# Performance work log

Measured on AMD Instinct MI355X. Metric: run time of the kernel, lower is better.

## Reference

```python
import jax, jax.numpy as jnp
import numpy as np

B, D_MODEL, H, D_MEM, M = 512, 2048, 8, 128, 512
MAX_WRITE_FACTOR = 0.7


def act(x):
    # elu(x) + 1, the standard positive linear-attention kernel activation
    return jax.nn.elu(x) + 1.0


def setup_inputs() -> dict:
    key = jax.random.key(0)
    ks = jax.random.split(key, 9)
    s = 1.0 / np.sqrt(D_MODEL)
    return {
        "key": jax.random.normal(ks[0], (B, D_MODEL), jnp.float32),
        "values": jax.random.normal(ks[1], (B, D_MODEL), jnp.float32),
        "memories": jax.random.normal(ks[2], (B, M, D_MEM), jnp.float32),
        "write_mass": jax.random.uniform(ks[3], (B, M, D_MEM), jnp.float32),
        "batch_mask": jnp.zeros((B,), jnp.bool_),
        "W_key": jax.random.normal(ks[4], (D_MODEL, H * D_MEM), jnp.float32) * s,
        "b_key": jnp.zeros((H * D_MEM,), jnp.float32),
        "W_val": jax.random.normal(ks[5], (D_MODEL, 2 * H * D_MEM), jnp.float32) * s,
        "b_val": jnp.zeros((2 * H * D_MEM,), jnp.float32),
        "addresses": jax.random.normal(ks[6], (M, D_MEM), jnp.float32),
        "interpolation_logits": jax.random.normal(ks[7], (M, D_MEM), jnp.float32),
    }


def reference(key, values, memories, write_mass, batch_mask,
              W_key, b_key, W_val, b_val, addresses, interpolation_logits):
    # project write heads
    k = (key @ W_key + b_key).reshape(B, H, D_MEM)            # (B, H, Dm)
    v = (values @ W_val + b_val).reshape(B, H, 2 * D_MEM)     # (B, H, 2Dm)

    # linear attention kernel over heads (items = H)
    ak = act(k)
    matrix = jnp.einsum('bhd,bhe->bde', ak, v)                 # (B, Dm, 2Dm)
    normalizer = jnp.sum(ak, axis=1)                           # (B, Dm)

    # read with memory addresses as queries
    aq = act(addresses)                                        # (M, Dm)
    numerator = jnp.einsum('md,bde->bme', aq, matrix)          # (B, M, 2Dm)
    denominator = jnp.einsum('md,bd->bm', aq, normalizer) + 1e-5
    results = numerator / denominator[..., None]

    update = results[..., :D_MEM]                              # (B, M, Dm)
    write_logits = results[..., D_MEM:]                        # (B, M, Dm)

    write_probability = jax.nn.sigmoid(write_logits)
    interpolation_factor = jax.nn.sigmoid(interpolation_logits)  # (M, Dm)
    write_factor = MAX_WRITE_FACTOR * write_probability * interpolation_factor

    # probability-gated EMA-style commit
    next_memories = memories * (1.0 - write_factor) + update * write_factor
    next_mass = write_mass + write_factor

    mask = batch_mask[:, None, None]
    next_memories = jnp.where(mask, memories, next_memories)
    next_mass = jnp.where(mask, write_mass, next_mass)
    return next_memories, next_mass
```

## Files before the change

### kernel.cpp

```cpp
#include <hip/hip_runtime.h>


typedef _Float16 half8  __attribute__((ext_vector_type(8)));
typedef _Float16 half4v __attribute__((ext_vector_type(4)));
typedef float    f32x4  __attribute__((ext_vector_type(4)));

#define NB      512
#define DMODEL  2048
#define NH      8
#define DMEM    128
#define NM      512
#define NMTOT   33554432

__device__ __forceinline__ f32x4 ntload4(const float* p) {
    return __builtin_nontemporal_load((const f32x4*)p);
}
__device__ __forceinline__ void ntstore4(float* p, f32x4 v) {
    __builtin_nontemporal_store(v, (f32x4*)p);
}

__global__ void prep_all(const float* __restrict__ key, const float* __restrict__ values,
                         const float* __restrict__ addresses, const float* __restrict__ ilog,
                         _Float16* __restrict__ key16, _Float16* __restrict__ val16,
                         float* __restrict__ aqF, _Float16* __restrict__ aqH,
                         float* __restrict__ sigI) {
    const int bid = blockIdx.x;
    if (bid < 2048) {
        const float* src = (bid < 1024) ? key : values;
        _Float16* dst = (bid < 1024) ? key16 : val16;
        int i = (bid & 1023) * 256 + threadIdx.x;
        float4 v = ((const float4*)src)[i];
        half4v o;
        o[0] = (_Float16)v.x; o[1] = (_Float16)v.y;
        o[2] = (_Float16)v.z; o[3] = (_Float16)v.w;
        ((half4v*)dst)[i] = o;
    } else {
        int i = (bid - 2048) * 256 + threadIdx.x;
        float a = addresses[i];
        float v = a > 0.f ? a + 1.f : __expf(a);
        aqF[i] = v;
        aqH[i] = (_Float16)v;
        sigI[i] = 1.0f / (1.0f + __expf(-ilog[i]));
    }
}

__global__ void transp_cvt(const float* __restrict__ W, _Float16* __restrict__ Wt, int N) {
    __shared__ float tile[32][33];
    const int k0 = blockIdx.x * 32, n0 = blockIdx.y * 32;
    const int c = threadIdx.x & 31, r0 = threadIdx.x >> 5;
#pragma unroll
    for (int i = 0; i < 4; i++) {
        int r = r0 + i * 8;
        tile[r][c] = W[(size_t)(k0 + r) * N + n0 + c];
    }
    __syncthreads();
#pragma unroll
    for (int i = 0; i < 4; i++) {
        int r = r0 + i * 8;
        Wt[(size_t)(n0 + r) * 2048 + k0 + c] = (_Float16)tile[c][r];
    }
}

__global__ __launch_bounds__(256) void gemm_kv(
        const _Float16* __restrict__ key16,
        const _Float16* __restrict__ val16,
        const _Float16* __restrict__ WkT,
        const _Float16* __restrict__ WvT,
        const float* __restrict__ b_key,
        const float* __restrict__ b_val,
        float* __restrict__ akF,
        _Float16* __restrict__ vH) {
    __shared__ _Float16 As[2][64][72];
    __shared__ _Float16 Bs[2][64][72];

    const int t = threadIdx.x;
    const int m0 = blockIdx.x * 64;
    const int n0 = blockIdx.y * 64;
    const bool isK = (n0 < 1024);
    const _Float16* aSrc = isK ? key16 : val16;
    const _Float16* bSrc = isK ? (WkT + (size_t)n0 * 2048)
                               : (WvT + (size_t)(n0 - 1024) * 2048);

    const int w = t >> 6, lane = t & 63;
    const int col = lane & 15, q = lane >> 4;
    const int wm = (w & 1) * 32, wn = (w >> 1) * 32;

    const int row0 = t >> 3, ch = t & 7;
    const int row1 = (t + 256) >> 3;

    f32x4 acc[2][2];
#pragma unroll
    for (int i = 0; i < 2; i++)
#pragma unroll
        for (int j = 0; j < 2; j++) acc[i][j] = (f32x4){0.f, 0.f, 0.f, 0.f};

    uint4 ra0 = *(const uint4*)(aSrc + (size_t)(m0 + row0) * 2048 + ch * 8);
    uint4 ra1 = *(const uint4*)(aSrc + (size_t)(m0 + row1) * 2048 + ch * 8);
    uint4 rb0 = *(const uint4*)(bSrc + (size_t)row0 * 2048 + ch * 8);
    uint4 rb1 = *(const uint4*)(bSrc + (size_t)row1 * 2048 + ch * 8);

    int buf = 0;
    for (int k0 = 0; k0 < 2048; k0 += 64) {
        *(uint4*)&As[buf][row0][ch * 8] = ra0;
        *(uint4*)&As[buf][row1][ch * 8] = ra1;
        *(uint4*)&Bs[buf][row0][ch * 8] = rb0;
        *(uint4*)&Bs[buf][row1][ch * 8] = rb1;
        if (k0 + 64 < 2048) {
            const int kn = k0 + 64;
            ra0 = *(const uint4*)(aSrc + (size_t)(m0 + row0) * 2048 + kn + ch * 8);
            ra1 = *(const uint4*)(aSrc + (size_t)(m0 + row1) * 2048 + kn + ch * 8);
            rb0 = *(const uint4*)(bSrc + (size_t)row0 * 2048 + kn + ch * 8);
            rb1 = *(const uint4*)(bSrc + (size_t)row1 * 2048 + kn + ch * 8);
        }
        __syncthreads();
#pragma unroll
        for (int ks = 0; ks < 2; ks++) {
            half8 a0 = *(const half8*)&As[buf][wm + col][ks * 32 + q * 8];
            half8 a1 = *(const half8*)&As[buf][wm + 16 + col][ks * 32 + q * 8];
            half8 b0 = *(const half8*)&Bs[buf][wn + col][ks * 32 + q * 8];
            half8 b1 = *(const half8*)&Bs[buf][wn + 16 + col][ks * 32 + q * 8];
            acc[0][0] = __builtin_amdgcn_mfma_f32_16x16x32_f16(a0, b0, acc[0][0], 0, 0, 0);
            acc[0][1] = __builtin_amdgcn_mfma_f32_16x16x32_f16(a0, b1, acc[0][1], 0, 0, 0);
            acc[1][0] = __builtin_amdgcn_mfma_f32_16x16x32_f16(a1, b0, acc[1][0], 0, 0, 0);
            acc[1][1] = __builtin_amdgcn_mfma_f32_16x16x32_f16(a1, b1, acc[1][1], 0, 0, 0);
        }
        buf ^= 1;
    }
#pragma unroll
    for (int mt = 0; mt < 2; mt++) {
#pragma unroll
        for (int nt = 0; nt < 2; nt++) {
            int n = n0 + wn + nt * 16 + col;
#pragma unroll
            for (int r = 0; r < 4; r++) {
                int m = m0 + wm + mt * 16 + q * 4 + r;
                float x = acc[mt][nt][r];
                if (isK) {
                    x += b_key[n];
                    akF[(size_t)m * 1024 + n] = (x > 0.f) ? (x + 1.f) : __expf(x);
                } else {
                    int nn = n - 1024;
                    x += b_val[nn];
                    vH[(size_t)m * 2048 + nn] = (_Float16)x;
                }
            }
        }
    }
}

struct MWBuf { f32x4 pm[2]; f32x4 pw[2]; };
struct PSBuf { f32x4 ps[2]; };

__global__ __launch_bounds__(512, 4) void fused_mem(
    const float* __restrict__ akF,
    const _Float16* __restrict__ vH,
    const _Float16* __restrict__ aqH,
    const float* __restrict__ aqF,
    const float* __restrict__ sigI,
    const float* __restrict__ memories,
    const float* __restrict__ write_mass,
    const unsigned char* __restrict__ bmask,
    float* __restrict__ out) {
    __shared__ _Float16 matT[128][DMEM + 8];
    __shared__ float    uT[64][68];
    __shared__ float    gT[64][68];
    __shared__ float    sA[NH][DMEM];
    __shared__ _Float16 sV[NH][128];
    __shared__ float    sNrm[DMEM];
    __shared__ float    sDen[NM];

    const int b  = blockIdx.x;
    const int eh = blockIdx.y;
    const int t = threadIdx.x;
    const int w = t >> 6, lane = t & 63;
    const int col = lane & 15, q = lane >> 4;
    const int wq = w >> 1, slice = w & 1;
    const size_t obase = (size_t)b * (NM * DMEM);
    const int ebase = eh * 64;

    auto issue_mw = [&](MWBuf& pb, int s) {
        const int it = s >> 2, mt = s & 3;
        const int e4 = ebase + (lane & 15) * 4;
#pragma unroll
        for (int p = 0; p < 2; p++) {
            const int x = w * 8 + p * 4 + (lane >> 4);
            const int m = (x >> 4) * 64 + it * 256 + mt * 16 + (x & 15);
            const size_t gi = (size_t)m * 128 + e4;
            pb.pm[p] = ntload4(memories + obase + gi);
            pb.pw[p] = ntload4(write_mass + obase + gi);
        }
    };
    auto issue_ps = [&](PSBuf& pb, int s) {
        const int it = s >> 2, mt = s & 3;
        const int e4 = ebase + (lane & 15) * 4;
#pragma unroll
        for (int p = 0; p < 2; p++) {
            const int x = w * 8 + p * 4 + (lane >> 4);
            const int m = (x >> 4) * 64 + it * 256 + mt * 16 + (x & 15);
            pb.ps[p] = *(const f32x4*)(sigI + (size_t)m * 128 + e4);
        }
    };

    MWBuf M0, M1, M2;
    PSBuf S0, S1;

    issue_mw(M0, 0);
    issue_ps(S0, 0);
    issue_mw(M1, 1);

    if (t < 256) {
        ((float4*)&sA[0][0])[t] = ((const float4*)(akF + (size_t)b * 1024))[t];
    }
    if (t < 128) {
        const int h = t >> 4, grp = t & 15;
        const int eg = (grp < 8) ? (ebase + grp * 8) : (128 + ebase + (grp - 8) * 8);
        *(half8*)&sV[h][grp * 8] = *(const half8*)(vH + (size_t)b * 2048 + h * 256 + eg);
    }
    __syncthreads();

    if (t < 128) {
        float s = 0.f;
#pragma unroll
        for (int h = 0; h < NH; h++) s += sA[h][t];
        sNrm[t] = s;
    }

    {
        const int d0 = (t & 31) * 4;
        const int e0 = (t >> 5) * 8;
        float c[8][4];
#pragma unroll
        for (int e = 0; e < 8; e++)
#pragma unroll
            for (int d = 0; d < 4; d++) c[e][d] = 0.f;
#pragma unroll
        for (int h = 0; h < NH; h++) {
            float4 av = *(const float4*)&sA[h][d0];
            half8 vv = *(const half8*)&sV[h][e0];
#pragma unroll
            for (int e = 0; e < 8; e++) {
                float vf = (float)vv[e];
                c[e][0] += av.x * vf; c[e][1] += av.y * vf;
                c[e][2] += av.z * vf; c[e][3] += av.w * vf;
            }
        }
#pragma unroll
        for (int e = 0; e < 8; e++) {
            half4v o;
            o[0] = (_Float16)c[e][0]; o[1] = (_Float16)c[e][1];
            o[2] = (_Float16)c[e][2]; o[3] = (_Float16)c[e][3];
            *(half4v*)&matT[e0 + e][d0] = o;
        }
    }
    __syncthreads();

    {
        const int l32 = lane & 31;
        const int hh = lane >> 5;
        const float4 nv = *(const float4*)&sNrm[l32 * 4];
#pragma unroll 4
        for (int pass = 0; pass < 32; pass++) {
            int m = pass * 16 + w * 2 + hh;
            float4 qv = *(const float4*)(aqF + (size_t)m * 128 + l32 * 4);
            float s = qv.x * nv.x + qv.y * nv.y + qv.z * nv.z + qv.w * nv.w;
            s += __shfl_xor(s, 1);  s += __shfl_xor(s, 2);  s += __shfl_xor(s, 4);
            s += __shfl_xor(s, 8);  s += __shfl_xor(s, 16);
            if (l32 == 0) sDen[m] = 1.0f / (s + 1e-5f);
        }
    }
    __syncthreads();

    const float wfscale = (bmask[b] != 0) ? 0.0f : 0.7f;

    auto do_step = [&](int s, MWBuf& cm, PSBuf& cs, MWBuf& nm, PSBuf& ns) {
        if (s + 2 < 8) issue_mw(nm, s + 2);
        if (s + 1 < 8) issue_ps(ns, s + 1);

        const int it = s >> 2, mt = s & 3;
        const int mrowBase = (wq + it * 4) * 64 + mt * 16;
        f32x4 acc[4];
#pragma unroll
        for (int nt = 0; nt < 4; nt++) acc[nt] = (f32x4){0.f, 0.f, 0.f, 0.f};
#pragma unroll
        for (int ks = 0; ks < 4; ks++) {
            const half8 af = *(const half8*)(aqH + (size_t)(mrowBase + col) * 128
                                             + ks * 32 + q * 8);
#pragma unroll
            for (int nt = 0; nt < 4; nt++) {
                const half8 bf = *(const half8*)&matT[(nt >> 1) * 64 + slice * 32
                                                      + (nt & 1) * 16 + col]
                                                     [ks * 32 + q * 8];
                acc[nt] = __builtin_amdgcn_mfma_f32_16x16x32_f16(af, bf, acc[nt], 0, 0, 0);
            }
        }

        asm volatile("s_waitcnt lgkmcnt(0)" ::: "memory");
        __builtin_amdgcn_s_barrier();
        __builtin_amdgcn_sched_barrier(0);

        const int r0 = wq * 16 + q * 4;
#pragma unroll
        for (int r = 0; r < 4; r++) {
            uT[r0 + r][slice * 32 + col]      = acc[0][r];
            uT[r0 + r][slice * 32 + 16 + col] = acc[1][r];
            gT[r0 + r][slice * 32 + col]      = acc[2][r];
            gT[r0 + r][slice * 32 + 16 + col] = acc[3][r];
        }

        asm volatile("s_waitcnt lgkmcnt(0)" ::: "memory");
        __builtin_amdgcn_s_barrier();
        __builtin_amdgcn_sched_barrier(0);

        const int e4l = (lane & 15) * 4;
#pragma unroll
        for (int p = 0; p < 2; p++) {
            const int x = w * 8 + p * 4 + (lane >> 4);
            const int m = (x >> 4) * 64 + it * 256 + mt * 16 + (x & 15);
            const f32x4 u = *(const f32x4*)&uT[x][e4l];
            const f32x4 g = *(const f32x4*)&gT[x][e4l];
            const float rc = sDen[m];
            const size_t gi = obase + (size_t)m * 128 + ebase + e4l;
            f32x4 o1, o2;
#pragma unroll
            for (int j = 0; j < 4; j++) {
                const float upd = u[j] * rc;
                const float wl  = g[j] * rc;
                const float wpb = 1.0f / (1.0f + __expf(-wl));
                const float wf  = wfscale * wpb * cs.ps[p][j];
                o1[j] = cm.pm[p][j] + wf * (upd - cm.pm[p][j]);
                o2[j] = cm.pw[p][j] + wf;
            }
            ntstore4(out + gi, o1);
            ntstore4(out + NMTOT + gi, o2);
        }
    };

    do_step(0, M0, S0, M2, S1);
    do_step(1, M1, S1, M0, S0);
    do_step(2, M2, S0, M1, S1);
    do_step(3, M0, S1, M2, S0);
    do_step(4, M1, S0, M0, S1);
    do_step(5, M2, S1, M1, S0);
    do_step(6, M0, S0, M2, S1);
    do_step(7, M1, S1, M0, S0);
}

extern "C" void kernel_launch(void* const* d_in, const int* in_sizes, int n_in,
                              void* d_out, int out_size, void* d_ws, size_t ws_size,
                              hipStream_t stream) {
    const float* key        = (const float*)d_in[0];
    const float* values     = (const float*)d_in[1];
    const float* memories   = (const float*)d_in[2];
    const float* write_mass = (const float*)d_in[3];
    const unsigned char* bm = (const unsigned char*)d_in[4];
    const float* W_key      = (const float*)d_in[5];
    const float* b_key      = (const float*)d_in[6];
    const float* W_val      = (const float*)d_in[7];
    const float* b_val      = (const float*)d_in[8];
    const float* addresses  = (const float*)d_in[9];
    const float* ilog       = (const float*)d_in[10];
    float* out = (float*)d_out;

    char* ws = (char*)d_ws;
    _Float16* key16 = (_Float16*)ws;  ws += (size_t)512 * 2048 * 2;
    _Float16* val16 = (_Float16*)ws;  ws += (size_t)512 * 2048 * 2;
    _Float16* WkT   = (_Float16*)ws;  ws += (size_t)1024 * 2048 * 2;
    _Float16* WvT   = (_Float16*)ws;  ws += (size_t)2048 * 2048 * 2;
    float*    akF   = (float*)ws;     ws += (size_t)512 * 1024 * 4;
    _Float16* vH    = (_Float16*)ws;  ws += (size_t)512 * 2048 * 2;
    float*    aqF   = (float*)ws;     ws += (size_t)512 * 128 * 4;
    _Float16* aqH   = (_Float16*)ws;  ws += (size_t)512 * 128 * 2;
    float*    sigI  = (float*)ws;     ws += (size_t)512 * 128 * 4;

    prep_all<<<2304, 256, 0, stream>>>(key, values, addresses, ilog,
                                       key16, val16, aqF, aqH, sigI);
    transp_cvt<<<dim3(64, 32), 256, 0, stream>>>(W_key, WkT, 1024);
    transp_cvt<<<dim3(64, 64), 256, 0, stream>>>(W_val, WvT, 2048);
    gemm_kv<<<dim3(8, 48), 256, 0, stream>>>(key16, val16, WkT, WvT, b_key, b_val, akF, vH);
    fused_mem<<<dim3(512, 2), 512, 0, stream>>>(akF, vH, aqH, aqF, sigI, memories, write_mass, bm, out);
}
```

Before: 561.9 us.

## Give each wave its own 64 memory rows and drop block-wide barriers in fused_mem

Each wave now owns a contiguous 64-row slab of memory slots and computes all 128 output columns (update and gate) for its 16-row tiles. Results are transposed through a per-wave LDS scratch that is synchronized only with wave barriers, so the two block-wide barriers per step are gone. The explicit multi-stage register prefetch of memories, write_mass and sigI is dropped. Loads are now issued at the top of each step and the compiler is relied on to overlap them with the MFMAs, which risks exposing more memory latency. Each wave does twice as many MFMAs per step, which raises register pressure.

```diff
diff --git a/kernel.cpp b/kernel.cpp
--- a/kernel.cpp
+++ b/kernel.cpp
@@ -148,9 +148,6 @@
     }
 }
 
-struct MWBuf { f32x4 pm[2]; f32x4 pw[2]; };
-struct PSBuf { f32x4 ps[2]; };
-
 __global__ __launch_bounds__(512, 4) void fused_mem(
     const float* __restrict__ akF,
     const _Float16* __restrict__ vH,
@@ -162,8 +159,7 @@
     const unsigned char* __restrict__ bmask,
     float* __restrict__ out) {
     __shared__ _Float16 matT[128][DMEM + 8];
-    __shared__ float    uT[64][68];
-    __shared__ float    gT[64][68];
+    __shared__ float    wsT[8][16][68];
     __shared__ float    sA[NH][DMEM];
     __shared__ _Float16 sV[NH][128];
     __shared__ float    sNrm[DMEM];
@@ -174,39 +170,11 @@
     const int t = threadIdx.x;
     const int w = t >> 6, lane = t & 63;
     const int col = lane & 15, q = lane >> 4;
-    const int wq = w >> 1, slice = w & 1;
     const size_t obase = (size_t)b * (NM * DMEM);
     const int ebase = eh * 64;
 
-    auto issue_mw = [&](MWBuf& pb, int s) {
-        const int it = s >> 2, mt = s & 3;
-        const int e4 = ebase + (lane & 15) * 4;
-#pragma unroll
-        for (int p = 0; p < 2; p++) {
-            const int x = w * 8 + p * 4 + (lane >> 4);
-            const int m = (x >> 4) * 64 + it * 256 + mt * 16 + (x & 15);
-            const size_t gi = (size_t)m * 128 + e4;
-            pb.pm[p] = ntload4(memories + obase + gi);
-            pb.pw[p] = ntload4(write_mass + obase + gi);
-        }
-    };
-    auto issue_ps = [&](PSBuf& pb, int s) {
-        const int it = s >> 2, mt = s & 3;
-        const int e4 = ebase + (lane & 15) * 4;
-#pragma unroll
-        for (int p = 0; p < 2; p++) {
-            const int x = w * 8 + p * 4 + (lane >> 4);
-            const int m = (x >> 4) * 64 + it * 256 + mt * 16 + (x & 15);
-            pb.ps[p] = *(const f32x4*)(sigI + (size_t)m * 128 + e4);
-        }
-    };
-
-    MWBuf M0, M1, M2;
-    PSBuf S0, S1;
-
-    issue_mw(M0, 0);
-    issue_ps(S0, 0);
-    issue_mw(M1, 1);
+    const int rr = lane >> 4;
+    const int c4 = (lane & 15) * 4;
 
     if (t < 256) {
         ((float4*)&sA[0][0])[t] = ((const float4*)(akF + (size_t)b * 1024))[t];
@@ -271,78 +239,82 @@
     __syncthreads();
 
     const float wfscale = (bmask[b] != 0) ? 0.0f : 0.7f;
-
-    auto do_step = [&](int s, MWBuf& cm, PSBuf& cs, MWBuf& nm, PSBuf& ns) {
-        if (s + 2 < 8) issue_mw(nm, s + 2);
-        if (s + 1 < 8) issue_ps(ns, s + 1);
-
-        const int it = s >> 2, mt = s & 3;
-        const int mrowBase = (wq + it * 4) * 64 + mt * 16;
-        f32x4 acc[4];
-#pragma unroll
-        for (int nt = 0; nt < 4; nt++) acc[nt] = (f32x4){0.f, 0.f, 0.f, 0.f};
+    float (*ws)[68] = wsT[w];
+    const int mwave = w * 64;
+
+#pragma unroll 1
+    for (int s = 0; s < 4; s++) {
+        const int mbase = mwave + s * 16;
+
+        f32x4 pm[4], pw[4];
+#pragma unroll
+        for (int j = 0; j < 4; j++) {
+            const size_t gi = obase + (size_t)(mbase + rr + 4 * j) * 128 + ebase + c4;
+            pm[j] = ntload4(memories + gi);
+            pw[j] = ntload4(write_mass + gi);
+        }
+
+        f32x4 acc[2][4];
+#pragma unroll
+        for (int h = 0; h < 2; h++)
+#pragma unroll
+            for (int nt = 0; nt < 4; nt++) acc[h][nt] = (f32x4){0.f, 0.f, 0.f, 0.f};
 #pragma unroll
         for (int ks = 0; ks < 4; ks++) {
-            const half8 af = *(const half8*)(aqH + (size_t)(mrowBase + col) * 128
+            const half8 af = *(const half8*)(aqH + (size_t)(mbase + col) * 128
                                              + ks * 32 + q * 8);
 #pragma unroll
-            for (int nt = 0; nt < 4; nt++) {
-                const half8 bf = *(const half8*)&matT[(nt >> 1) * 64 + slice * 32
-                                                      + (nt & 1) * 16 + col]
-                                                     [ks * 32 + q * 8];
-                acc[nt] = __builtin_amdgcn_mfma_f32_16x16x32_f16(af, bf, acc[nt], 0, 0, 0);
-            }
-        }
-
-        asm volatile("s_waitcnt lgkmcnt(0)" ::: "memory");
-        __builtin_amdgcn_s_barrier();
-        __builtin_amdgcn_sched_barrier(0);
-
-        const int r0 = wq * 16 + q * 4;
-#pragma unroll
-        for (int r = 0; r < 4; r++) {
-            uT[r0 + r][slice * 32 + col]      = acc[0][r];
-            uT[r0 + r][slice * 32 + 16 + col] = acc[1][r];
-            gT[r0 + r][slice * 32 + col]      = acc[2][r];
-            gT[r0 + r][slice * 32 + 16 + col] = acc[3][r];
-        }
-
-        asm volatile("s_waitcnt lgkmcnt(0)" ::: "memory");
-        __builtin_amdgcn_s_barrier();
-        __builtin_amdgcn_sched_barrier(0);
-
-        const int e4l = (lane & 15) * 4;
-#pragma unroll
-        for (int p = 0; p < 2; p++) {
-            const int x = w * 8 + p * 4 + (lane >> 4);
-            const int m = (x >> 4) * 64 + it * 256 + mt * 16 + (x & 15);
-            const f32x4 u = *(const f32x4*)&uT[x][e4l];
-            const f32x4 g = *(const f32x4*)&gT[x][e4l];
+            for (int h = 0; h < 2; h++)
+#pragma unroll
+                for (int nt = 0; nt < 4; nt++) {
+                    const half8 bf = *(const half8*)&matT[h * 64 + nt * 16 + col]
+                                                         [ks * 32 + q * 8];
+                    acc[h][nt] = __builtin_amdgcn_mfma_f32_16x16x32_f16(af, bf,
+                                                                        acc[h][nt], 0, 0, 0);
+                }
+        }
+
+#pragma unroll
+        for (int r = 0; r < 4; r++)
+#pragma unroll
+            for (int nt = 0; nt < 4; nt++)
+                ws[q * 4 + r][nt * 16 + col] = acc[0][nt][r];
+        __builtin_amdgcn_wave_barrier();
+        f32x4 u[4];
+#pragma unroll
+        for (int j = 0; j < 4; j++) u[j] = *(const f32x4*)&ws[rr + 4 * j][c4];
+        __builtin_amdgcn_wave_barrier();
+#pragma unroll
+        for (int r = 0; r < 4; r++)
+#pragma unroll
+            for (int nt = 0; nt < 4; nt++)
+                ws[q * 4 + r][nt * 16 + col] = acc[1][nt][r];
+        __builtin_amdgcn_wave_barrier();
+        f32x4 g[4];
+#pragma unroll
+        for (int j = 0; j < 4; j++) g[j] = *(const f32x4*)&ws[rr + 4 * j][c4];
+        __builtin_amdgcn_wave_barrier();
+
+#pragma unroll
+        for (int j = 0; j < 4; j++) {
+            const int m = mbase + rr + 4 * j;
             const float rc = sDen[m];
-            const size_t gi = obase + (size_t)m * 128 + ebase + e4l;
+            const f32x4 si = *(const f32x4*)(sigI + (size_t)m * 128 + ebase + c4);
+            const size_t gi = obase + (size_t)m * 128 + ebase + c4;
             f32x4 o1, o2;
 #pragma unroll
-            for (int j = 0; j < 4; j++) {
-                const float upd = u[j] * rc;
-                const float wl  = g[j] * rc;
+            for (int jj = 0; jj < 4; jj++) {
+                const float upd = u[j][jj] * rc;
+                const float wl  = g[j][jj] * rc;
                 const float wpb = 1.0f / (1.0f + __expf(-wl));
-                const float wf  = wfscale * wpb * cs.ps[p][j];
-                o1[j] = cm.pm[p][j] + wf * (upd - cm.pm[p][j]);
-                o2[j] = cm.pw[p][j] + wf;
+                const float wf  = wfscale * wpb * si[jj];
+                o1[jj] = pm[j][jj] + wf * (upd - pm[j][jj]);
+                o2[jj] = pw[j][jj] + wf;
             }
             ntstore4(out + gi, o1);
             ntstore4(out + NMTOT + gi, o2);
         }
-    };
-
-    do_step(0, M0, S0, M2, S1);
-    do_step(1, M1, S1, M0, S0);
-    do_step(2, M2, S0, M1, S1);
-    do_step(3, M0, S1, M2, S0);
-    do_step(4, M1, S0, M0, S1);
-    do_step(5, M2, S1, M1, S0);
-    do_step(6, M0, S0, M2, S1);
-    do_step(7, M1, S1, M0, S0);
+    }
 }
 
 extern "C" void kernel_launch(void* const* d_in, const int* in_sizes, int n_in,
```

New measurement: 537.1 us. 1.05x faster.
